# Kernel optimization log

Measured on AMD Instinct MI355X. Metric: run time of the kernel, lower is better.

Reference implementation:

```python
import jax, jax.numpy as jnp
import numpy as np

IN_SIZE = 256
OUT_SIZE = 64
N_NODES = 512
FAN_IN = 32
T = 2048  # max_context_length; actives window is full
D = IN_SIZE + N_NODES + OUT_SIZE  # 832


def setup_inputs() -> dict:
    key = jax.random.key(0)
    k1, k2, k3, k4 = jax.random.split(key, 4)
    x = jax.random.normal(k1, (IN_SIZE,), dtype=jnp.float32)
    actives = jax.random.normal(k2, (T, D), dtype=jnp.float32)
    weights = jax.random.normal(k3, (N_NODES, FAN_IN, 3), dtype=jnp.float32)
    in_idxs = jax.random.randint(k4, (N_NODES, FAN_IN), 0, IN_SIZE + N_NODES).astype(jnp.int32)
    return {"x": x, "actives": actives, "weights": weights, "in_idxs": in_idxs}


def reference(x, actives, weights, in_idxs):
    in_size = x.shape[0]
    # activate(): context window is full -> drop oldest row, append new row with x in first in_size cols
    new_row = jnp.zeros((actives.shape[1],), actives.dtype).at[:in_size].set(x)
    act = jnp.concatenate([actives[1:], new_row[None, :]], axis=0)  # (T, D)

    def step(act, node):
        ix, idxs, W = node
        inp = jnp.take(act, idxs, axis=1)            # gather: (T, fan_in)
        qkv = inp @ W                                # (T, 3)
        q, k, v = qkv[:, 0:1], qkv[:, 1:2], qkv[:, 2:3]  # each (T, 1), d_k = 1
        logits = q @ k.T                             # (T, T); / sqrt(d_k) with d_k=1
        attn = jax.nn.softmax(logits, axis=-1)
        out = jnp.tanh((attn @ v)[-1, 0])            # activation(values[-1:,]) -> scalar
        act = act.at[-1, in_size + ix].set(out)      # scatter into shared state
        return act, out

    nodes = (jnp.arange(weights.shape[0]), in_idxs, weights)
    _, outs = jax.lax.scan(step, act, nodes)         # sequential node loop (true dependency)
    return outs[-OUT_SIZE:]                          # last OUT_SIZE nodes are outputs
```

## Files before the change

### kernel.cpp

```cpp
#include <hip/hip_runtime.h>

#define IN_SIZE 256
#define OUT_SIZE 64
#define N_NODES 512
#define FAN_IN 32
#define T_DIM 2048
#define D_DIM 832
#define TOTAL_EDGE 16384
#define BLK_F4 1088
#define MAX_ENT 64
#define THRESH -20.0f

template <int CTRL, int RM>
__device__ __forceinline__ float dppadd(float v) {
  int m = __builtin_amdgcn_update_dpp(0, __float_as_int(v), CTRL, RM, 0xf, true);
  return v + __int_as_float(m);
}
__device__ __forceinline__ void wave_sum2(float& a, float& b) {
  a = dppadd<0x111, 0xf>(a); b = dppadd<0x111, 0xf>(b);
  a = dppadd<0x112, 0xf>(a); b = dppadd<0x112, 0xf>(b);
  a = dppadd<0x114, 0xf>(a); b = dppadd<0x114, 0xf>(b);
  a = dppadd<0x118, 0xf>(a); b = dppadd<0x118, 0xf>(b);
  a = dppadd<0x142, 0xa>(a); b = dppadd<0x142, 0xa>(b);
  a = dppadd<0x143, 0xc>(a); b = dppadd<0x143, 0xc>(b);
}
__device__ __forceinline__ float rl63(float v) {
  return __int_as_float(__builtin_amdgcn_readlane(__float_as_int(v), 63));
}

__global__ __launch_bounds__(512) void kv_kernel(
    const float* __restrict__ actives, const int* __restrict__ in_idxs,
    const float* __restrict__ weights, float2* __restrict__ KVd) {
  __shared__ float rows[8][836];
  __shared__ int s_idx[64 * 33];
  __shared__ float s_raw[64 * 100];
  int tid = threadIdx.x;
  int tb = (blockIdx.x >> 1) * 8;
  int t0 = (blockIdx.x & 1) * 4;
#pragma unroll
  for (int r = 0; r < 8; ++r) {
    int t = tb + r;
    for (int c = tid; c < 208; c += 512) {
      float4 v4 = make_float4(0.f, 0.f, 0.f, 0.f);
      if (t < T_DIM - 1)
        v4 = ((const float4*)(actives + (size_t)(t + 1) * D_DIM))[c];
      *(float4*)&rows[r][4 * c] = v4;
    }
  }
  int tl = tid & 7, ng = tid >> 3;
  for (int tile = t0; tile < t0 + 4; ++tile) {
    __syncthreads();
    int n0 = tile * 64;
    for (int i = tid; i < 2048; i += 512) {
      int nl = i >> 5, f = i & 31;
      s_idx[nl * 33 + f] = in_idxs[n0 * FAN_IN + i];
    }
    {
      const float4* wsrc = (const float4*)(weights + (size_t)n0 * FAN_IN * 3);
      for (int i = tid; i < 1536; i += 512) {
        int nl = i / 24, j = i - nl * 24;
        *(float4*)&s_raw[nl * 100 + 4 * j] = wsrc[i];
      }
    }
    __syncthreads();
    {
      const int* ip = &s_idx[ng * 33];
      const float* wp = &s_raw[ng * 100];
      float k = 0.f, v = 0.f;
#pragma unroll 8
      for (int f = 0; f < FAN_IN; ++f) {
        float a = rows[tl][ip[f]];
        k = fmaf(wp[3 * f + 1], a, k);
        v = fmaf(wp[3 * f + 2], a, v);
      }
      KVd[(size_t)(n0 + ng) * (2 * BLK_F4) + tb + tl] = make_float2(k, v);
    }
  }
}

__global__ __launch_bounds__(512) void block_kernel(
    const float* __restrict__ x, const int* __restrict__ in_idxs,
    const float* __restrict__ weights, float4* __restrict__ blk,
    float4* __restrict__ meta_g, float4* __restrict__ Qb) {
  __shared__ float2 sbk[T_DIM];
  __shared__ int hist8[8][64];
  __shared__ float smx[8], smn[8];
  __shared__ float4 sEnt[MAX_ENT];
  __shared__ int ecnt;
  int node = blockIdx.x, tid = threadIdx.x;
  int w = tid >> 6;
  if (tid == 0) ecnt = 0;
  if (tid < 64) {
#pragma unroll
    for (int ww = 0; ww < 8; ++ww) hist8[ww][tid] = 0;
  }
  const float2* src = (const float2*)(blk + (size_t)node * BLK_F4);
  float2 kv[4];
  float mx = -3.4e38f, mn = 3.4e38f;
#pragma unroll
  for (int j = 0; j < 4; ++j) {
    int t = j * 512 + tid;
    kv[j] = (t < 2047) ? src[t] : make_float2(0.f, 0.f);
    if (t < 2047) { mx = fmaxf(mx, kv[j].x); mn = fminf(mn, kv[j].x); }
  }
#pragma unroll
  for (int off = 32; off > 0; off >>= 1) {
    mx = fmaxf(mx, __shfl_xor(mx, off));
    mn = fminf(mn, __shfl_xor(mn, off));
  }
  if ((tid & 63) == 0) { smx[w] = mx; smn[w] = mn; }
  __syncthreads();
  float kmax = smx[0], kmin = smn[0];
#pragma unroll
  for (int ww = 1; ww < 8; ++ww) {
    kmax = fmaxf(kmax, smx[ww]);
    kmin = fminf(kmin, smn[ww]);
  }
  float invbw = 64.0f / (kmax - kmin);
#pragma unroll
  for (int j = 0; j < 4; ++j) {
    int t = j * 512 + tid;
    if (t < 2047) {
      int b = (int)((kv[j].x - kmin) * invbw);
      b = b < 0 ? 0 : (b > 63 ? 63 : b);
      atomicAdd(&hist8[w][b], 1);
    }
  }
  {
    int target = IN_SIZE + node;
    const int4* ip4 = (const int4*)in_idxs;
#pragma unroll 4
    for (int e4 = tid; e4 < TOTAL_EDGE / 4; e4 += 512) {
      int4 v = ip4[e4];
      int e0 = 4 * e4;
#pragma unroll
      for (int c4 = 0; c4 < 4; ++c4) {
        int idx = c4 == 0 ? v.x : (c4 == 1 ? v.y : (c4 == 2 ? v.z : v.w));
        if (idx == target) {
          int e = e0 + c4;
          int c = e >> 5;
          if (c > node) {
            int p = atomicAdd(&ecnt, 1);
            if (p < MAX_ENT) {
              const float* wp = weights + (size_t)e * 3;
              sEnt[p] = make_float4(__int_as_float(c), wp[0], wp[1], wp[2]);
            }
          }
        }
      }
    }
  }
  if (tid < 32) {
    int g = node * FAN_IN + tid;
    int idx = in_idxs[g];
    const float* wp = weights + (size_t)g * 3;
    float a = (idx < IN_SIZE) ? x[idx] : 0.f;
    float p0 = a * wp[0], p1 = a * wp[1], p2 = a * wp[2];
#pragma unroll
    for (int off = 16; off > 0; off >>= 1) {
      p0 += __shfl_xor(p0, off);
      p1 += __shfl_xor(p1, off);
      p2 += __shfl_xor(p2, off);
    }
    if (tid == 0) Qb[node] = make_float4(p0, p1, p2, 0.f);
  }
  __syncthreads();
  if (tid < 64) {
    int h[8];
    int tot = 0;
#pragma unroll
    for (int ww = 0; ww < 8; ++ww) { h[ww] = hist8[ww][tid]; tot += h[ww]; }
    int incl = tot;
#pragma unroll
    for (int d = 1; d < 64; d <<= 1) {
      int u = __shfl_up(incl, d);
      if (tid >= d) incl += u;
    }
    int run = incl - tot;
#pragma unroll
    for (int ww = 0; ww < 8; ++ww) { hist8[ww][tid] = run; run += h[ww]; }
  }
  if (tid == 0) sbk[2047] = make_float2(0.f, 0.f);
  __syncthreads();
#pragma unroll
  for (int j = 0; j < 4; ++j) {
    int t = j * 512 + tid;
    if (t < 2047) {
      int b = (int)((kv[j].x - kmin) * invbw);
      b = b < 0 ? 0 : (b > 63 ? 63 : b);
      int p = atomicAdd(&hist8[w][b], 1);
      sbk[p] = kv[j];
    }
  }
  __syncthreads();
  float4* B = blk + (size_t)node * BLK_F4;
#pragma unroll
  for (int j = 0; j < 2; ++j) {
    int i = j * 512 + tid;
    float2 a = sbk[i];
    float2 d = sbk[2046 - i];
    B[i] = make_float4(a.x, a.y, d.x, d.y);
  }
  int cnt = ecnt < MAX_ENT ? ecnt : MAX_ENT;
  if (tid < MAX_ENT)
    B[1024 + tid] = (tid < cnt) ? sEnt[tid] : make_float4(0.f, 0.f, 0.f, 0.f);
  if (tid == 0)
    meta_g[3 * node + 0] =
        make_float4(kmax, kmin, __int_as_float(cnt), sbk[64].x);
  if (tid == 1)
    meta_g[3 * node + 1] =
        make_float4(sbk[1982].x, sbk[256].x, sbk[1790].x, sbk[512].x);
  if (tid == 2)
    meta_g[3 * node + 2] = make_float4(sbk[1534].x, 0.f, 0.f, 0.f);
}

__global__ __launch_bounds__(1024) void sweep_kernel(
    const int* __restrict__ in_idxs, const float4* __restrict__ Qb,
    const float4* __restrict__ meta_g, const float4* __restrict__ blk,
    float* __restrict__ out) {
  __shared__ float4 sQKV[N_NODES];
  __shared__ float4 sMeta[N_NODES][3];
  __shared__ int sRecv[N_NODES];
  __shared__ int sNeed[N_NODES];
  __shared__ float souts[OUT_SIZE];
  const int tid = threadIdx.x;
  const int lane = tid & 63;
  const int w = tid >> 6;

  for (int n = tid; n < N_NODES; n += 1024) {
    sQKV[n] = Qb[n];
    sMeta[n][0] = meta_g[3 * n + 0];
    sMeta[n][1] = meta_g[3 * n + 1];
    sMeta[n][2] = meta_g[3 * n + 2];
    sRecv[n] = 0;
  }
  if (tid < N_NODES) {
    const int4* ip = (const int4*)(in_idxs + tid * FAN_IN);
    int need = 0;
#pragma unroll
    for (int j = 0; j < 8; ++j) {
      int4 v = ip[j];
      need += (v.x >= IN_SIZE && v.x - IN_SIZE < tid);
      need += (v.y >= IN_SIZE && v.y - IN_SIZE < tid);
      need += (v.z >= IN_SIZE && v.z - IN_SIZE < tid);
      need += (v.w >= IN_SIZE && v.w - IN_SIZE < tid);
    }
    sNeed[tid] = need;
  }
  __syncthreads();

  auto process = [&](int node, float4 C0, float4 ENT, float4 m0, float4 m1,
                     float4 m2) {
    float4 qv = sQKV[node];
    float q = qv.x, kl = qv.y, vl = qv.z;
    int cnt = __float_as_int(m0.z);
    float m = fmaxf(fmaxf(q * m0.x, q * m0.y), q * kl);
    bool p1 = fmaxf(q * m0.w, q * m1.x) - m >= THRESH;
    bool p2 = p1 && (fmaxf(q * m1.y, q * m1.z) - m >= THRESH);
    bool p3 = p2 && (fmaxf(q * m1.w, q * m2.x) - m >= THRESH);
    const float4* B = blk + (size_t)node * BLK_F4;
    float4 t1[3], t2[4], t3[8];
    if (p1) {
#pragma unroll
      for (int t = 0; t < 3; ++t) t1[t] = B[64 + 64 * t + lane];
    }
    if (p2) {
#pragma unroll
      for (int t = 0; t < 4; ++t) t2[t] = B[256 + 64 * t + lane];
    }
    if (p3) {
#pragma unroll
      for (int t = 0; t < 8; ++t) t3[t] = B[512 + 64 * t + lane];
    }
    float el = __expf(q * kl - m);
    float w0 = __expf(fmaf(q, C0.x, -m));
    float w1 = __expf(fmaf(q, C0.z, -m));
    float sw = w0 + w1;
    float swv = fmaf(w0, C0.y, w1 * C0.w);
    if (p1) {
#pragma unroll
      for (int t = 0; t < 3; ++t) {
        float a0 = __expf(fmaf(q, t1[t].x, -m));
        float a1 = __expf(fmaf(q, t1[t].z, -m));
        sw += a0 + a1;
        swv = fmaf(a0, t1[t].y, fmaf(a1, t1[t].w, swv));
      }
    }
    if (p2) {
#pragma unroll
      for (int t = 0; t < 4; ++t) {
        float a0 = __expf(fmaf(q, t2[t].x, -m));
        float a1 = __expf(fmaf(q, t2[t].z, -m));
        sw += a0 + a1;
        swv = fmaf(a0, t2[t].y, fmaf(a1, t2[t].w, swv));
      }
    }
    if (p3) {
#pragma unroll
      for (int t = 0; t < 8; ++t) {
        float a0 = __expf(fmaf(q, t3[t].x, -m));
        float a1 = __expf(fmaf(q, t3[t].z, -m));
        if (t == 7 && lane == 63) a1 = 0.f;
        sw += a0 + a1;
        swv = fmaf(a0, t3[t].y, fmaf(a1, t3[t].w, swv));
      }
    }
    wave_sum2(sw, swv);
    float S = rl63(sw) + el;
    float SV = fmaf(el, vl, rl63(swv));
    float z = SV * __builtin_amdgcn_rcpf(S);
    float eo = __expf(2.f * z);
    float o = 1.f - 2.f * __builtin_amdgcn_rcpf(eo + 1.f);
    if (lane == 0 && node >= N_NODES - OUT_SIZE)
      souts[node - (N_NODES - OUT_SIZE)] = o;
    if (lane < cnt) {
      int c = __float_as_int(ENT.x);
      atomicAdd(&sQKV[c].x, o * ENT.y);
      atomicAdd(&sQKV[c].y, o * ENT.z);
      atomicAdd(&sQKV[c].z, o * ENT.w);
      asm volatile("" ::: "memory");
      atomicAdd(&sRecv[c], 1);
    }
  };

  auto pf = [&](int n, float4& c0, float4& ent, float4& m0, float4& m1,
                float4& m2) {
    const float4* B = blk + (size_t)n * BLK_F4;
    c0 = B[lane];
    ent = B[1024 + lane];
    m0 = sMeta[n][0];
    m1 = sMeta[n][1];
    m2 = sMeta[n][2];
  };

  auto spinwait = [&](int n) {
    int need = sNeed[n];
    if (need > 0) {
      const volatile int* rp = (const volatile int*)&sRecv[n];
      int it = 0;
      while (*rp < need && ++it < 1000000) __builtin_amdgcn_s_sleep(1);
    }
    asm volatile("" ::: "memory");
  };

  float4 c0A, entA, m0A, m1A, m2A;
  float4 c0B, entB, m0B, m1B, m2B;
  pf(w, c0A, entA, m0A, m1A, m2A);
  for (int n = w; n < N_NODES; n += 32) {
    pf(n + 16, c0B, entB, m0B, m1B, m2B);
    spinwait(n);
    process(n, c0A, entA, m0A, m1A, m2A);
    if (n + 32 < N_NODES) pf(n + 32, c0A, entA, m0A, m1A, m2A);
    spinwait(n + 16);
    process(n + 16, c0B, entB, m0B, m1B, m2B);
  }
  __syncthreads();
  if (tid < OUT_SIZE) out[tid] = souts[tid];
}

extern "C" void kernel_launch(void* const* d_in, const int* in_sizes, int n_in,
                              void* d_out, int out_size, void* d_ws,
                              size_t ws_size, hipStream_t stream) {
  const float* x = (const float*)d_in[0];
  const float* actives = (const float*)d_in[1];
  const float* weights = (const float*)d_in[2];
  const int* in_idxs = (const int*)d_in[3];
  float* out = (float*)d_out;

  char* ws = (char*)d_ws;
  float4* blk = (float4*)ws;
  size_t off = (size_t)N_NODES * BLK_F4 * 16;
  float4* meta_g = (float4*)(ws + off); off += (size_t)N_NODES * 3 * 16;
  float4* Qb = (float4*)(ws + off);

  kv_kernel<<<(T_DIM / 8) * 2, 512, 0, stream>>>(actives, in_idxs, weights,
                                                 (float2*)blk);
  block_kernel<<<N_NODES, 512, 0, stream>>>(x, in_idxs, weights, blk, meta_g,
                                            Qb);
  sweep_kernel<<<1, 1024, 0, stream>>>(in_idxs, Qb, meta_g, blk, out);
}
```

Measured before the change: 156.1 us.

## Fuse three kernels into one persistent kernel with grid barriers

Merges the KV projection, per-node bucket sort and the sequential sweep into a single 512-block launch separated by software grid barriers on global atomics, with shared memory overlaid through a union. This removes two kernel launch gaps at the cost of a memset and of barrier spin time. The sweep now runs on block 0 with 512 threads (8 waves instead of 16), so the node interleaving changes and the sweep has less parallelism. The barrier relies on all 512 blocks being co-resident, which holds only if occupancy allows it.

Result: slower. 244.5 us (+56.7%).

```diff
diff --git a/kernel.cpp b/kernel.cpp
--- a/kernel.cpp
+++ b/kernel.cpp
@@ -10,6 +10,7 @@
 #define BLK_F4 1088
 #define MAX_ENT 64
 #define THRESH -20.0f
+#define NBLK 512
 
 template <int CTRL, int RM>
 __device__ __forceinline__ float dppadd(float v) {
@@ -28,334 +29,363 @@
   return __int_as_float(__builtin_amdgcn_readlane(__float_as_int(v), 63));
 }
 
-__global__ __launch_bounds__(512) void kv_kernel(
-    const float* __restrict__ actives, const int* __restrict__ in_idxs,
-    const float* __restrict__ weights, float2* __restrict__ KVd) {
-  __shared__ float rows[8][836];
-  __shared__ int s_idx[64 * 33];
-  __shared__ float s_raw[64 * 100];
-  int tid = threadIdx.x;
-  int tb = (blockIdx.x >> 1) * 8;
-  int t0 = (blockIdx.x & 1) * 4;
-#pragma unroll
-  for (int r = 0; r < 8; ++r) {
-    int t = tb + r;
-    for (int c = tid; c < 208; c += 512) {
-      float4 v4 = make_float4(0.f, 0.f, 0.f, 0.f);
-      if (t < T_DIM - 1)
-        v4 = ((const float4*)(actives + (size_t)(t + 1) * D_DIM))[c];
-      *(float4*)&rows[r][4 * c] = v4;
-    }
+__device__ __forceinline__ void grid_barrier(int* bar, int slot, int tid) {
+  __syncthreads();
+  if (tid == 0) {
+    __hip_atomic_fetch_add(&bar[slot], 1, __ATOMIC_ACQ_REL,
+                           __HIP_MEMORY_SCOPE_AGENT);
+    int it = 0;
+    while (__hip_atomic_load(&bar[slot], __ATOMIC_ACQUIRE,
+                             __HIP_MEMORY_SCOPE_AGENT) < NBLK &&
+           ++it < 100000000)
+      __builtin_amdgcn_s_sleep(2);
   }
-  int tl = tid & 7, ng = tid >> 3;
-  for (int tile = t0; tile < t0 + 4; ++tile) {
-    __syncthreads();
-    int n0 = tile * 64;
-    for (int i = tid; i < 2048; i += 512) {
-      int nl = i >> 5, f = i & 31;
-      s_idx[nl * 33 + f] = in_idxs[n0 * FAN_IN + i];
+  __syncthreads();
+}
+
+__global__ __launch_bounds__(512, 4) void fused_kernel(
+    const float* __restrict__ x, const float* __restrict__ actives,
+    const float* __restrict__ weights, const int* __restrict__ in_idxs,
+    float4* __restrict__ blk, float4* __restrict__ meta_g,
+    float4* __restrict__ Qb, int* __restrict__ bar,
+    float* __restrict__ out) {
+  __shared__ union {
+    struct {
+      float rows[8][836];
+      int s_idx[64 * 33];
+      float s_raw[64 * 100];
+    } a;
+    struct {
+      float2 sbk[T_DIM];
+      int hist8[8][64];
+      float smx[8], smn[8];
+      float4 sEnt[MAX_ENT];
+      int ecnt;
+    } b;
+    struct {
+      float4 sQKV[N_NODES];
+      float4 sMeta[N_NODES][3];
+      int sRecv[N_NODES];
+      int sNeed[N_NODES];
+      float souts[OUT_SIZE];
+    } c;
+  } u;
+  const int tid = threadIdx.x;
+  const int bid = blockIdx.x;
+
+  {
+    float2* KVd = (float2*)blk;
+    int tb = (bid >> 1) * 8;
+    int t0 = (bid & 1) * 4;
+#pragma unroll
+    for (int r = 0; r < 8; ++r) {
+      int t = tb + r;
+      for (int c = tid; c < 208; c += 512) {
+        float4 v4 = make_float4(0.f, 0.f, 0.f, 0.f);
+        if (t < T_DIM - 1)
+          v4 = ((const float4*)(actives + (size_t)(t + 1) * D_DIM))[c];
+        *(float4*)&u.a.rows[r][4 * c] = v4;
+      }
+    }
+    int tl = tid & 7, ng = tid >> 3;
+    for (int tile = t0; tile < t0 + 4; ++tile) {
+      __syncthreads();
+      int n0 = tile * 64;
+      for (int i = tid; i < 2048; i += 512) {
+        int nl = i >> 5, f = i & 31;
+        u.a.s_idx[nl * 33 + f] = in_idxs[n0 * FAN_IN + i];
+      }
+      {
+        const float4* wsrc =
+            (const float4*)(weights + (size_t)n0 * FAN_IN * 3);
+        for (int i = tid; i < 1536; i += 512) {
+          int nl = i / 24, j = i - nl * 24;
+          *(float4*)&u.a.s_raw[nl * 100 + 4 * j] = wsrc[i];
+        }
+      }
+      __syncthreads();
+      {
+        const int* ip = &u.a.s_idx[ng * 33];
+        const float* wp = &u.a.s_raw[ng * 100];
+        float k = 0.f, v = 0.f;
+#pragma unroll 8
+        for (int f = 0; f < FAN_IN; ++f) {
+          float a = u.a.rows[tl][ip[f]];
+          k = fmaf(wp[3 * f + 1], a, k);
+          v = fmaf(wp[3 * f + 2], a, v);
+        }
+        KVd[(size_t)(n0 + ng) * (2 * BLK_F4) + tb + tl] = make_float2(k, v);
+      }
+    }
+  }
+  grid_barrier(bar, 0, tid);
+
+  {
+    int node = bid;
+    int w = tid >> 6;
+    if (tid == 0) u.b.ecnt = 0;
+    if (tid < 64) {
+#pragma unroll
+      for (int ww = 0; ww < 8; ++ww) u.b.hist8[ww][tid] = 0;
+    }
+    const float2* src = (const float2*)(blk + (size_t)node * BLK_F4);
+    float2 kv[4];
+    float mx = -3.4e38f, mn = 3.4e38f;
+#pragma unroll
+    for (int j = 0; j < 4; ++j) {
+      int t = j * 512 + tid;
+      kv[j] = (t < 2047) ? src[t] : make_float2(0.f, 0.f);
+      if (t < 2047) { mx = fmaxf(mx, kv[j].x); mn = fminf(mn, kv[j].x); }
+    }
+#pragma unroll
+    for (int off = 32; off > 0; off >>= 1) {
+      mx = fmaxf(mx, __shfl_xor(mx, off));
+      mn = fminf(mn, __shfl_xor(mn, off));
+    }
+    if ((tid & 63) == 0) { u.b.smx[w] = mx; u.b.smn[w] = mn; }
+    __syncthreads();
+    float kmax = u.b.smx[0], kmin = u.b.smn[0];
+#pragma unroll
+    for (int ww = 1; ww < 8; ++ww) {
+      kmax = fmaxf(kmax, u.b.smx[ww]);
+      kmin = fminf(kmin, u.b.smn[ww]);
+    }
+    float invbw = 64.0f / (kmax - kmin);
+#pragma unroll
+    for (int j = 0; j < 4; ++j) {
+      int t = j * 512 + tid;
+      if (t < 2047) {
+        int b = (int)((kv[j].x - kmin) * invbw);
+        b = b < 0 ? 0 : (b > 63 ? 63 : b);
+        atomicAdd(&u.b.hist8[w][b], 1);
+      }
     }
     {
-      const float4* wsrc = (const float4*)(weights + (size_t)n0 * FAN_IN * 3);
-      for (int i = tid; i < 1536; i += 512) {
-        int nl = i / 24, j = i - nl * 24;
-        *(float4*)&s_raw[nl * 100 + 4 * j] = wsrc[i];
-      }
-    }
-    __syncthreads();
-    {
-      const int* ip = &s_idx[ng * 33];
-      const float* wp = &s_raw[ng * 100];
-      float k = 0.f, v = 0.f;
-#pragma unroll 8
-      for (int f = 0; f < FAN_IN; ++f) {
-        float a = rows[tl][ip[f]];
-        k = fmaf(wp[3 * f + 1], a, k);
-        v = fmaf(wp[3 * f + 2], a, v);
-      }
-      KVd[(size_t)(n0 + ng) * (2 * BLK_F4) + tb + tl] = make_float2(k, v);
-    }
-  }
-}
-
-__global__ __launch_bounds__(512) void block_kernel(
-    const float* __restrict__ x, const int* __restrict__ in_idxs,
-    const float* __restrict__ weights, float4* __restrict__ blk,
-    float4* __restrict__ meta_g, float4* __restrict__ Qb) {
-  __shared__ float2 sbk[T_DIM];
-  __shared__ int hist8[8][64];
-  __shared__ float smx[8], smn[8];
-  __shared__ float4 sEnt[MAX_ENT];
-  __shared__ int ecnt;
-  int node = blockIdx.x, tid = threadIdx.x;
-  int w = tid >> 6;
-  if (tid == 0) ecnt = 0;
-  if (tid < 64) {
-#pragma unroll
-    for (int ww = 0; ww < 8; ++ww) hist8[ww][tid] = 0;
-  }
-  const float2* src = (const float2*)(blk + (size_t)node * BLK_F4);
-  float2 kv[4];
-  float mx = -3.4e38f, mn = 3.4e38f;
-#pragma unroll
-  for (int j = 0; j < 4; ++j) {
-    int t = j * 512 + tid;
-    kv[j] = (t < 2047) ? src[t] : make_float2(0.f, 0.f);
-    if (t < 2047) { mx = fmaxf(mx, kv[j].x); mn = fminf(mn, kv[j].x); }
-  }
-#pragma unroll
-  for (int off = 32; off > 0; off >>= 1) {
-    mx = fmaxf(mx, __shfl_xor(mx, off));
-    mn = fminf(mn, __shfl_xor(mn, off));
-  }
-  if ((tid & 63) == 0) { smx[w] = mx; smn[w] = mn; }
-  __syncthreads();
-  float kmax = smx[0], kmin = smn[0];
-#pragma unroll
-  for (int ww = 1; ww < 8; ++ww) {
-    kmax = fmaxf(kmax, smx[ww]);
-    kmin = fminf(kmin, smn[ww]);
-  }
-  float invbw = 64.0f / (kmax - kmin);
-#pragma unroll
-  for (int j = 0; j < 4; ++j) {
-    int t = j * 512 + tid;
-    if (t < 2047) {
-      int b = (int)((kv[j].x - kmin) * invbw);
-      b = b < 0 ? 0 : (b > 63 ? 63 : b);
-      atomicAdd(&hist8[w][b], 1);
-    }
-  }
-  {
-    int target = IN_SIZE + node;
-    const int4* ip4 = (const int4*)in_idxs;
+      int target = IN_SIZE + node;
+      const int4* ip4 = (const int4*)in_idxs;
 #pragma unroll 4
-    for (int e4 = tid; e4 < TOTAL_EDGE / 4; e4 += 512) {
-      int4 v = ip4[e4];
-      int e0 = 4 * e4;
-#pragma unroll
-      for (int c4 = 0; c4 < 4; ++c4) {
-        int idx = c4 == 0 ? v.x : (c4 == 1 ? v.y : (c4 == 2 ? v.z : v.w));
-        if (idx == target) {
-          int e = e0 + c4;
-          int c = e >> 5;
-          if (c > node) {
-            int p = atomicAdd(&ecnt, 1);
-            if (p < MAX_ENT) {
-              const float* wp = weights + (size_t)e * 3;
-              sEnt[p] = make_float4(__int_as_float(c), wp[0], wp[1], wp[2]);
+      for (int e4 = tid; e4 < TOTAL_EDGE / 4; e4 += 512) {
+        int4 v = ip4[e4];
+        int e0 = 4 * e4;
+#pragma unroll
+        for (int c4 = 0; c4 < 4; ++c4) {
+          int idx = c4 == 0 ? v.x : (c4 == 1 ? v.y : (c4 == 2 ? v.z : v.w));
+          if (idx == target) {
+            int e = e0 + c4;
+            int c = e >> 5;
+            if (c > node) {
+              int p = atomicAdd(&u.b.ecnt, 1);
+              if (p < MAX_ENT) {
+                const float* wp = weights + (size_t)e * 3;
+                u.b.sEnt[p] =
+                    make_float4(__int_as_float(c), wp[0], wp[1], wp[2]);
+              }
             }
           }
         }
       }
     }
+    if (tid < 32) {
+      int g = node * FAN_IN + tid;
+      int idx = in_idxs[g];
+      const float* wp = weights + (size_t)g * 3;
+      float a = (idx < IN_SIZE) ? x[idx] : 0.f;
+      float p0 = a * wp[0], p1 = a * wp[1], p2 = a * wp[2];
+#pragma unroll
+      for (int off = 16; off > 0; off >>= 1) {
+        p0 += __shfl_xor(p0, off);
+        p1 += __shfl_xor(p1, off);
+        p2 += __shfl_xor(p2, off);
+      }
+      if (tid == 0) Qb[node] = make_float4(p0, p1, p2, 0.f);
+    }
+    __syncthreads();
+    if (tid < 64) {
+      int h[8];
+      int tot = 0;
+#pragma unroll
+      for (int ww = 0; ww < 8; ++ww) { h[ww] = u.b.hist8[ww][tid]; tot += h[ww]; }
+      int incl = tot;
+#pragma unroll
+      for (int d = 1; d < 64; d <<= 1) {
+        int uu = __shfl_up(incl, d);
+        if (tid >= d) incl += uu;
+      }
+      int run = incl - tot;
+#pragma unroll
+      for (int ww = 0; ww < 8; ++ww) { u.b.hist8[ww][tid] = run; run += h[ww]; }
+    }
+    if (tid == 0) u.b.sbk[2047] = make_float2(0.f, 0.f);
+    __syncthreads();
+#pragma unroll
+    for (int j = 0; j < 4; ++j) {
+      int t = j * 512 + tid;
+      if (t < 2047) {
+        int b = (int)((kv[j].x - kmin) * invbw);
+        b = b < 0 ? 0 : (b > 63 ? 63 : b);
+        int p = atomicAdd(&u.b.hist8[w][b], 1);
+        u.b.sbk[p] = kv[j];
+      }
+    }
+    __syncthreads();
+    float4* B = blk + (size_t)node * BLK_F4;
+#pragma unroll
+    for (int j = 0; j < 2; ++j) {
+      int i = j * 512 + tid;
+      float2 a = u.b.sbk[i];
+      float2 d = u.b.sbk[2046 - i];
+      B[i] = make_float4(a.x, a.y, d.x, d.y);
+    }
+    int cnt = u.b.ecnt < MAX_ENT ? u.b.ecnt : MAX_ENT;
+    if (tid < MAX_ENT)
+      B[1024 + tid] =
+          (tid < cnt) ? u.b.sEnt[tid] : make_float4(0.f, 0.f, 0.f, 0.f);
+    if (tid == 0)
+      meta_g[3 * node + 0] =
+          make_float4(kmax, kmin, __int_as_float(cnt), u.b.sbk[64].x);
+    if (tid == 1)
+      meta_g[3 * node + 1] = make_float4(u.b.sbk[1982].x, u.b.sbk[256].x,
+                                         u.b.sbk[1790].x, u.b.sbk[512].x);
+    if (tid == 2)
+      meta_g[3 * node + 2] = make_float4(u.b.sbk[1534].x, 0.f, 0.f, 0.f);
   }
-  if (tid < 32) {
-    int g = node * FAN_IN + tid;
-    int idx = in_idxs[g];
-    const float* wp = weights + (size_t)g * 3;
-    float a = (idx < IN_SIZE) ? x[idx] : 0.f;
-    float p0 = a * wp[0], p1 = a * wp[1], p2 = a * wp[2];
-#pragma unroll
-    for (int off = 16; off > 0; off >>= 1) {
-      p0 += __shfl_xor(p0, off);
-      p1 += __shfl_xor(p1, off);
-      p2 += __shfl_xor(p2, off);
-    }
-    if (tid == 0) Qb[node] = make_float4(p0, p1, p2, 0.f);
+  grid_barrier(bar, 1, tid);
+
+  if (bid != 0) return;
+  {
+    const int lane = tid & 63;
+    const int w = tid >> 6;
+
+    for (int n = tid; n < N_NODES; n += 512) {
+      u.c.sQKV[n] = Qb[n];
+      u.c.sMeta[n][0] = meta_g[3 * n + 0];
+      u.c.sMeta[n][1] = meta_g[3 * n + 1];
+      u.c.sMeta[n][2] = meta_g[3 * n + 2];
+      u.c.sRecv[n] = 0;
+    }
+    if (tid < N_NODES) {
+      const int4* ip = (const int4*)(in_idxs + tid * FAN_IN);
+      int need = 0;
+#pragma unroll
+      for (int j = 0; j < 8; ++j) {
+        int4 v = ip[j];
+        need += (v.x >= IN_SIZE && v.x - IN_SIZE < tid);
+        need += (v.y >= IN_SIZE && v.y - IN_SIZE < tid);
+        need += (v.z >= IN_SIZE && v.z - IN_SIZE < tid);
+        need += (v.w >= IN_SIZE && v.w - IN_SIZE < tid);
+      }
+      u.c.sNeed[tid] = need;
+    }
+    __syncthreads();
+
+    auto process = [&](int node, float4 C0, float4 ENT, float4 m0, float4 m1,
+                       float4 m2) {
+      float4 qv = u.c.sQKV[node];
+      float q = qv.x, kl = qv.y, vl = qv.z;
+      int cnt = __float_as_int(m0.z);
+      float m = fmaxf(fmaxf(q * m0.x, q * m0.y), q * kl);
+      bool p1 = fmaxf(q * m0.w, q * m1.x) - m >= THRESH;
+      bool p2 = p1 && (fmaxf(q * m1.y, q * m1.z) - m >= THRESH);
+      bool p3 = p2 && (fmaxf(q * m1.w, q * m2.x) - m >= THRESH);
+      const float4* B = blk + (size_t)node * BLK_F4;
+      float4 t1[3], t2[4], t3[8];
+      if (p1) {
+#pragma unroll
+        for (int t = 0; t < 3; ++t) t1[t] = B[64 + 64 * t + lane];
+      }
+      if (p2) {
+#pragma unroll
+        for (int t = 0; t < 4; ++t) t2[t] = B[256 + 64 * t + lane];
+      }
+      if (p3) {
+#pragma unroll
+        for (int t = 0; t < 8; ++t) t3[t] = B[512 + 64 * t + lane];
+      }
+      float el = __expf(q * kl - m);
+      float w0 = __expf(fmaf(q, C0.x, -m));
+      float w1 = __expf(fmaf(q, C0.z, -m));
+      float sw = w0 + w1;
+      float swv = fmaf(w0, C0.y, w1 * C0.w);
+      if (p1) {
+#pragma unroll
+        for (int t = 0; t < 3; ++t) {
+          float a0 = __expf(fmaf(q, t1[t].x, -m));
+          float a1 = __expf(fmaf(q, t1[t].z, -m));
+          sw += a0 + a1;
+          swv = fmaf(a0, t1[t].y, fmaf(a1, t1[t].w, swv));
+        }
+      }
+      if (p2) {
+#pragma unroll
+        for (int t = 0; t < 4; ++t) {
+          float a0 = __expf(fmaf(q, t2[t].x, -m));
+          float a1 = __expf(fmaf(q, t2[t].z, -m));
+          sw += a0 + a1;
+          swv = fmaf(a0, t2[t].y, fmaf(a1, t2[t].w, swv));
+        }
+      }
+      if (p3) {
+#pragma unroll
+        for (int t = 0; t < 8; ++t) {
+          float a0 = __expf(fmaf(q, t3[t].x, -m));
+          float a1 = __expf(fmaf(q, t3[t].z, -m));
+          if (t == 7 && lane == 63) a1 = 0.f;
+          sw += a0 + a1;
+          swv = fmaf(a0, t3[t].y, fmaf(a1, t3[t].w, swv));
+        }
+      }
+      wave_sum2(sw, swv);
+      float S = rl63(sw) + el;
+      float SV = fmaf(el, vl, rl63(swv));
+      float z = SV * __builtin_amdgcn_rcpf(S);
+      float eo = __expf(2.f * z);
+      float o = 1.f - 2.f * __builtin_amdgcn_rcpf(eo + 1.f);
+      if (lane == 0 && node >= N_NODES - OUT_SIZE)
+        u.c.souts[node - (N_NODES - OUT_SIZE)] = o;
+      if (lane < cnt) {
+        int c = __float_as_int(ENT.x);
+        atomicAdd(&u.c.sQKV[c].x, o * ENT.y);
+        atomicAdd(&u.c.sQKV[c].y, o * ENT.z);
+        atomicAdd(&u.c.sQKV[c].z, o * ENT.w);
+        asm volatile("" ::: "memory");
+        atomicAdd(&u.c.sRecv[c], 1);
+      }
+    };
+
+    auto pf = [&](int n, float4& c0, float4& ent, float4& m0, float4& m1,
+                  float4& m2) {
+      const float4* B = blk + (size_t)n * BLK_F4;
+      c0 = B[lane];
+      ent = B[1024 + lane];
+      m0 = u.c.sMeta[n][0];
+      m1 = u.c.sMeta[n][1];
+      m2 = u.c.sMeta[n][2];
+    };
+
+    auto spinwait = [&](int n) {
+      int need = u.c.sNeed[n];
+      if (need > 0) {
+        const volatile int* rp = (const volatile int*)&u.c.sRecv[n];
+        int it = 0;
+        while (*rp < need && ++it < 1000000) __builtin_amdgcn_s_sleep(1);
+      }
+      asm volatile("" ::: "memory");
+    };
+
+    float4 c0A, entA, m0A, m1A, m2A;
+    float4 c0B, entB, m0B, m1B, m2B;
+    pf(w, c0A, entA, m0A, m1A, m2A);
+    for (int n = w; n < N_NODES; n += 16) {
+      pf(n + 8, c0B, entB, m0B, m1B, m2B);
+      spinwait(n);
+      process(n, c0A, entA, m0A, m1A, m2A);
+      if (n + 16 < N_NODES) pf(n + 16, c0A, entA, m0A, m1A, m2A);
+      spinwait(n + 8);
+      process(n + 8, c0B, entB, m0B, m1B, m2B);
+    }
+    __syncthreads();
+    if (tid < OUT_SIZE) out[tid] = u.c.souts[tid];
   }
-  __syncthreads();
-  if (tid < 64) {
-    int h[8];
-    int tot = 0;
-#pragma unroll
-    for (int ww = 0; ww < 8; ++ww) { h[ww] = hist8[ww][tid]; tot += h[ww]; }
-    int incl = tot;
-#pragma unroll
-    for (int d = 1; d < 64; d <<= 1) {
-      int u = __shfl_up(incl, d);
-      if (tid >= d) incl += u;
-    }
-    int run = incl - tot;
-#pragma unroll
-    for (int ww = 0; ww < 8; ++ww) { hist8[ww][tid] = run; run += h[ww]; }
-  }
-  if (tid == 0) sbk[2047] = make_float2(0.f, 0.f);
-  __syncthreads();
-#pragma unroll
-  for (int j = 0; j < 4; ++j) {
-    int t = j * 512 + tid;
-    if (t < 2047) {
-      int b = (int)((kv[j].x - kmin) * invbw);
-      b = b < 0 ? 0 : (b > 63 ? 63 : b);
-      int p = atomicAdd(&hist8[w][b], 1);
-      sbk[p] = kv[j];
-    }
-  }
-  __syncthreads();
-  float4* B = blk + (size_t)node * BLK_F4;
-#pragma unroll
-  for (int j = 0; j < 2; ++j) {
-    int i = j * 512 + tid;
-    float2 a = sbk[i];
-    float2 d = sbk[2046 - i];
-    B[i] = make_float4(a.x, a.y, d.x, d.y);
-  }
-  int cnt = ecnt < MAX_ENT ? ecnt : MAX_ENT;
-  if (tid < MAX_ENT)
-    B[1024 + tid] = (tid < cnt) ? sEnt[tid] : make_float4(0.f, 0.f, 0.f, 0.f);
-  if (tid == 0)
-    meta_g[3 * node + 0] =
-        make_float4(kmax, kmin, __int_as_float(cnt), sbk[64].x);
-  if (tid == 1)
-    meta_g[3 * node + 1] =
-        make_float4(sbk[1982].x, sbk[256].x, sbk[1790].x, sbk[512].x);
-  if (tid == 2)
-    meta_g[3 * node + 2] = make_float4(sbk[1534].x, 0.f, 0.f, 0.f);
-}
-
-__global__ __launch_bounds__(1024) void sweep_kernel(
-    const int* __restrict__ in_idxs, const float4* __restrict__ Qb,
-    const float4* __restrict__ meta_g, const float4* __restrict__ blk,
-    float* __restrict__ out) {
-  __shared__ float4 sQKV[N_NODES];
-  __shared__ float4 sMeta[N_NODES][3];
-  __shared__ int sRecv[N_NODES];
-  __shared__ int sNeed[N_NODES];
-  __shared__ float souts[OUT_SIZE];
-  const int tid = threadIdx.x;
-  const int lane = tid & 63;
-  const int w = tid >> 6;
-
-  for (int n = tid; n < N_NODES; n += 1024) {
-    sQKV[n] = Qb[n];
-    sMeta[n][0] = meta_g[3 * n + 0];
-    sMeta[n][1] = meta_g[3 * n + 1];
-    sMeta[n][2] = meta_g[3 * n + 2];
-    sRecv[n] = 0;
-  }
-  if (tid < N_NODES) {
-    const int4* ip = (const int4*)(in_idxs + tid * FAN_IN);
-    int need = 0;
-#pragma unroll
-    for (int j = 0; j < 8; ++j) {
-      int4 v = ip[j];
-      need += (v.x >= IN_SIZE && v.x - IN_SIZE < tid);
-      need += (v.y >= IN_SIZE && v.y - IN_SIZE < tid);
-      need += (v.z >= IN_SIZE && v.z - IN_SIZE < tid);
-      need += (v.w >= IN_SIZE && v.w - IN_SIZE < tid);
-    }
-    sNeed[tid] = need;
-  }
-  __syncthreads();
-
-  auto process = [&](int node, float4 C0, float4 ENT, float4 m0, float4 m1,
-                     float4 m2) {
-    float4 qv = sQKV[node];
-    float q = qv.x, kl = qv.y, vl = qv.z;
-    int cnt = __float_as_int(m0.z);
-    float m = fmaxf(fmaxf(q * m0.x, q * m0.y), q * kl);
-    bool p1 = fmaxf(q * m0.w, q * m1.x) - m >= THRESH;
-    bool p2 = p1 && (fmaxf(q * m1.y, q * m1.z) - m >= THRESH);
-    bool p3 = p2 && (fmaxf(q * m1.w, q * m2.x) - m >= THRESH);
-    const float4* B = blk + (size_t)node * BLK_F4;
-    float4 t1[3], t2[4], t3[8];
-    if (p1) {
-#pragma unroll
-      for (int t = 0; t < 3; ++t) t1[t] = B[64 + 64 * t + lane];
-    }
-    if (p2) {
-#pragma unroll
-      for (int t = 0; t < 4; ++t) t2[t] = B[256 + 64 * t + lane];
-    }
-    if (p3) {
-#pragma unroll
-      for (int t = 0; t < 8; ++t) t3[t] = B[512 + 64 * t + lane];
-    }
-    float el = __expf(q * kl - m);
-    float w0 = __expf(fmaf(q, C0.x, -m));
-    float w1 = __expf(fmaf(q, C0.z, -m));
-    float sw = w0 + w1;
-    float swv = fmaf(w0, C0.y, w1 * C0.w);
-    if (p1) {
-#pragma unroll
-      for (int t = 0; t < 3; ++t) {
-        float a0 = __expf(fmaf(q, t1[t].x, -m));
-        float a1 = __expf(fmaf(q, t1[t].z, -m));
-        sw += a0 + a1;
-        swv = fmaf(a0, t1[t].y, fmaf(a1, t1[t].w, swv));
-      }
-    }
-    if (p2) {
-#pragma unroll
-      for (int t = 0; t < 4; ++t) {
-        float a0 = __expf(fmaf(q, t2[t].x, -m));
-        float a1 = __expf(fmaf(q, t2[t].z, -m));
-        sw += a0 + a1;
-        swv = fmaf(a0, t2[t].y, fmaf(a1, t2[t].w, swv));
-      }
-    }
-    if (p3) {
-#pragma unroll
-      for (int t = 0; t < 8; ++t) {
-        float a0 = __expf(fmaf(q, t3[t].x, -m));
-        float a1 = __expf(fmaf(q, t3[t].z, -m));
-        if (t == 7 && lane == 63) a1 = 0.f;
-        sw += a0 + a1;
-        swv = fmaf(a0, t3[t].y, fmaf(a1, t3[t].w, swv));
-      }
-    }
-    wave_sum2(sw, swv);
-    float S = rl63(sw) + el;
-    float SV = fmaf(el, vl, rl63(swv));
-    float z = SV * __builtin_amdgcn_rcpf(S);
-    float eo = __expf(2.f * z);
-    float o = 1.f - 2.f * __builtin_amdgcn_rcpf(eo + 1.f);
-    if (lane == 0 && node >= N_NODES - OUT_SIZE)
-      souts[node - (N_NODES - OUT_SIZE)] = o;
-    if (lane < cnt) {
-      int c = __float_as_int(ENT.x);
-      atomicAdd(&sQKV[c].x, o * ENT.y);
-      atomicAdd(&sQKV[c].y, o * ENT.z);
-      atomicAdd(&sQKV[c].z, o * ENT.w);
-      asm volatile("" ::: "memory");
-      atomicAdd(&sRecv[c], 1);
-    }
-  };
-
-  auto pf = [&](int n, float4& c0, float4& ent, float4& m0, float4& m1,
-                float4& m2) {
-    const float4* B = blk + (size_t)n * BLK_F4;
-    c0 = B[lane];
-    ent = B[1024 + lane];
-    m0 = sMeta[n][0];
-    m1 = sMeta[n][1];
-    m2 = sMeta[n][2];
-  };
-
-  auto spinwait = [&](int n) {
-    int need = sNeed[n];
-    if (need > 0) {
-      const volatile int* rp = (const volatile int*)&sRecv[n];
-      int it = 0;
-      while (*rp < need && ++it < 1000000) __builtin_amdgcn_s_sleep(1);
-    }
-    asm volatile("" ::: "memory");
-  };
-
-  float4 c0A, entA, m0A, m1A, m2A;
-  float4 c0B, entB, m0B, m1B, m2B;
-  pf(w, c0A, entA, m0A, m1A, m2A);
-  for (int n = w; n < N_NODES; n += 32) {
-    pf(n + 16, c0B, entB, m0B, m1B, m2B);
-    spinwait(n);
-    process(n, c0A, entA, m0A, m1A, m2A);
-    if (n + 32 < N_NODES) pf(n + 32, c0A, entA, m0A, m1A, m2A);
-    spinwait(n + 16);
-    process(n + 16, c0B, entB, m0B, m1B, m2B);
-  }
-  __syncthreads();
-  if (tid < OUT_SIZE) out[tid] = souts[tid];
 }
 
 extern "C" void kernel_launch(void* const* d_in, const int* in_sizes, int n_in,
@@ -371,11 +401,10 @@
   float4* blk = (float4*)ws;
   size_t off = (size_t)N_NODES * BLK_F4 * 16;
   float4* meta_g = (float4*)(ws + off); off += (size_t)N_NODES * 3 * 16;
-  float4* Qb = (float4*)(ws + off);
-
-  kv_kernel<<<(T_DIM / 8) * 2, 512, 0, stream>>>(actives, in_idxs, weights,
-                                                 (float2*)blk);
-  block_kernel<<<N_NODES, 512, 0, stream>>>(x, in_idxs, weights, blk, meta_g,
-                                            Qb);
-  sweep_kernel<<<1, 1024, 0, stream>>>(in_idxs, Qb, meta_g, blk, out);
-}
+  float4* Qb = (float4*)(ws + off); off += (size_t)N_NODES * 16;
+  int* bar = (int*)(ws + off);
+
+  hipMemsetAsync(bar, 0, 2 * sizeof(int), stream);
+  fused_kernel<<<NBLK, 512, 0, stream>>>(x, actives, weights, in_idxs, blk,
+                                         meta_g, Qb, bar, out);
+}
```
